# Performance work log

Hardware: AMD Instinct MI355X
Metric: run time of the kernel (lower is better)

## Reference

```python
import jax, jax.numpy as jnp
import numpy as np

NUM_FEATURES = 256
NUM_PIDS = 5532
CQ_SIZE = 5000
N_NONID = 256
N = 2048
OIM_SCALAR = 30.0
MOMENTUM = 0.5


def _unit_rows(key, shape):
    v = jax.random.normal(key, shape, dtype=jnp.float32)
    return v / jnp.linalg.norm(v, axis=-1, keepdims=True)


def setup_inputs() -> dict:
    key = jax.random.key(0)
    ks = jax.random.split(key, 8)
    inputs = _unit_rows(ks[0], (N, NUM_FEATURES))
    targets = jax.random.randint(ks[1], (N,), 0, NUM_PIDS + 100, dtype=jnp.int32)
    belong_to_first_half = jax.random.randint(ks[2], (N,), 0, 2) > 0
    non_id_feat = _unit_rows(ks[3], (N_NONID, NUM_FEATURES))
    lut = _unit_rows(ks[4], (NUM_PIDS, NUM_FEATURES))
    cq = _unit_rows(ks[5], (CQ_SIZE, NUM_FEATURES))
    first_pos_sample = _unit_rows(ks[6], (NUM_PIDS, NUM_FEATURES))
    second_pos_sample = _unit_rows(ks[7], (NUM_PIDS, NUM_FEATURES))
    return {
        "inputs": inputs,
        "non_id_feat": non_id_feat,
        "lut": lut,
        "cq": cq,
        "first_pos_sample": first_pos_sample,
        "second_pos_sample": second_pos_sample,
        "targets": targets,
        "belong_to_first_half": belong_to_first_half,
        "header": 0,
    }


def reference(inputs, non_id_feat, lut, cq, first_pos_sample, second_pos_sample,
              targets, belong_to_first_half, header):
    # OIM forward: similarities against labeled LUT and [circular queue; non-id feats]
    out_labeled = inputs @ lut.T                                  # [N, num_pids]
    out_unlabeled = inputs @ jnp.concatenate([cq, non_id_feat], 0).T  # [N, cq+nonid]
    projected = jnp.concatenate([out_labeled, out_unlabeled], axis=1)
    return projected * OIM_SCALAR
```

## Files before the change

kernel.cpp:

```cpp
#include <hip/hip_runtime.h>
#include <hip/hip_bf16.h>
#include <stdint.h>
#include <stddef.h>

#define NUM_FEATURES 256
#define NUM_PIDS 5532
#define CQ_SIZE 5000
#define N_NONID 256
#define N_ROWS 2048
#define N_COLS (NUM_PIDS + CQ_SIZE + N_NONID)
#define OIM_SCALAR 30.0f

#define BM 128
#define BN 128
#define BK 32
#define KITERS (NUM_FEATURES / BK)

typedef __bf16 bf16_t;
typedef __bf16 bf16x4 __attribute__((ext_vector_type(4)));
typedef __bf16 bf16x8 __attribute__((ext_vector_type(8)));
typedef float f32x4 __attribute__((ext_vector_type(4)));

__global__ void detect_dtype(const void* __restrict__ A, int* __restrict__ flag) {
    const bf16_t* ab = (const bf16_t*)A;
    const int lane = threadIdx.x;
    float s = 0.0f;
    #pragma unroll
    for (int j = 0; j < 4; ++j) {
        float x = (float)ab[lane * 4 + j];
        s += x * x;
    }
    #pragma unroll
    for (int off = 32; off > 0; off >>= 1) s += __shfl_down(s, off, 64);
    if (lane == 0) flag[0] = (s > 0.75f && s < 1.25f) ? 1 : 0;
}

template <bool F32>
__device__ __forceinline__ void gemm_body(
    const char* __restrict__ A, const char* __restrict__ lut,
    const char* __restrict__ cq, const char* __restrict__ nonid,
    char* __restrict__ out, bf16_t* As, bf16_t* Bs)
{
    constexpr int ES = F32 ? 4 : 2;
    const int tid  = threadIdx.x;
    const int wid  = tid >> 6;
    const int lane = tid & 63;
    const int m0 = blockIdx.y * BM;
    const int n0 = blockIdx.x * BN;

    constexpr int NJ    = F32 ? 4 : 2;
    constexpr int RSTEP = F32 ? 32 : 64;
    const int srow = F32 ? (tid >> 3) : (tid >> 2);
    const int skk  = F32 ? ((tid & 7) * 4) : ((tid & 3) * 8);

    const char* arow[NJ];
    const char* brow[NJ];
    #pragma unroll
    for (int j = 0; j < NJ; ++j) {
        const int rm = m0 + srow + j * RSTEP;
        arow[j] = A + ((size_t)rm * NUM_FEATURES + skk) * ES;
        int r = n0 + srow + j * RSTEP;
        r = r < (N_COLS - 1) ? r : (N_COLS - 1);
        const char* src;
        if (r < NUM_PIDS)                 src = lut   + (size_t)r * NUM_FEATURES * ES;
        else if (r < NUM_PIDS + CQ_SIZE)  src = cq    + (size_t)(r - NUM_PIDS) * NUM_FEATURES * ES;
        else                              src = nonid + (size_t)(r - NUM_PIDS - CQ_SIZE) * NUM_FEATURES * ES;
        brow[j] = src + (size_t)skk * ES;
    }

    const int wave_m = (wid >> 1) * 64;
    const int wave_n = (wid & 1) * 64;
    const int fr = lane & 15;
    const int fk = (lane >> 4) * 8;

    f32x4 acc[4][4] = {};

    for (int kt = 0; kt < KITERS; ++kt) {
        #pragma unroll
        for (int j = 0; j < NJ; ++j) {
            const int ldix = (srow + j * RSTEP) * BK + skk;
            if constexpr (F32) {
                float4 av = *(const float4*)arow[j];
                float4 bv = *(const float4*)brow[j];
                bf16x4 ac = { (bf16_t)av.x, (bf16_t)av.y, (bf16_t)av.z, (bf16_t)av.w };
                bf16x4 bc = { (bf16_t)bv.x, (bf16_t)bv.y, (bf16_t)bv.z, (bf16_t)bv.w };
                *(bf16x4*)&As[ldix] = ac;
                *(bf16x4*)&Bs[ldix] = bc;
            } else {
                *(bf16x8*)&As[ldix] = *(const bf16x8*)arow[j];
                *(bf16x8*)&Bs[ldix] = *(const bf16x8*)brow[j];
            }
            arow[j] += BK * ES;
            brow[j] += BK * ES;
        }
        __syncthreads();

        bf16x8 af[4], bfr[4];
        #pragma unroll
        for (int t = 0; t < 4; ++t) {
            af[t]  = *(const bf16x8*)&As[(wave_m + t * 16 + fr) * BK + fk];
            bfr[t] = *(const bf16x8*)&Bs[(wave_n + t * 16 + fr) * BK + fk];
        }
        #pragma unroll
        for (int tm = 0; tm < 4; ++tm)
            #pragma unroll
            for (int tn = 0; tn < 4; ++tn)
                acc[tm][tn] = __builtin_amdgcn_mfma_f32_16x16x32_bf16(
                    af[tm], bfr[tn], acc[tm][tn], 0, 0, 0);
        __syncthreads();
    }

    #pragma unroll
    for (int tm = 0; tm < 4; ++tm) {
        const int row_base = m0 + wave_m + tm * 16 + (lane >> 4) * 4;
        #pragma unroll
        for (int tn = 0; tn < 4; ++tn) {
            const int col = n0 + wave_n + tn * 16 + (lane & 15);
            if (col < N_COLS) {
                #pragma unroll
                for (int i = 0; i < 4; ++i) {
                    float v = acc[tm][tn][i] * OIM_SCALAR;
                    if constexpr (F32)
                        ((float*)out)[(size_t)(row_base + i) * N_COLS + col] = v;
                    else
                        ((bf16_t*)out)[(size_t)(row_base + i) * N_COLS + col] = (bf16_t)v;
                }
            }
        }
    }
}

__global__ __launch_bounds__(256)
void oim_gemm_kernel(const void* __restrict__ A, const void* __restrict__ lut,
                     const void* __restrict__ cq, const void* __restrict__ nonid,
                     void* __restrict__ out, const int* __restrict__ flag) {
    __shared__ __align__(16) bf16_t As[BM * BK];
    __shared__ __align__(16) bf16_t Bs[BN * BK];
    if (flag[0]) {
        gemm_body<false>((const char*)A, (const char*)lut, (const char*)cq,
                         (const char*)nonid, (char*)out, As, Bs);
    } else {
        gemm_body<true>((const char*)A, (const char*)lut, (const char*)cq,
                        (const char*)nonid, (char*)out, As, Bs);
    }
}

extern "C" void kernel_launch(void* const* d_in, const int* in_sizes, int n_in,
                              void* d_out, int out_size, void* d_ws, size_t ws_size,
                              hipStream_t stream) {
    const void* inputs = d_in[0];
    const void* nonid  = d_in[1];
    const void* lut    = d_in[2];
    const void* cq     = d_in[3];
    int* flag = (int*)d_ws;

    detect_dtype<<<1, 64, 0, stream>>>(inputs, flag);

    dim3 grid((N_COLS + BN - 1) / BN, N_ROWS / BM);
    oim_gemm_kernel<<<grid, 256, 0, stream>>>(inputs, lut, cq, nonid, d_out, flag);
}
```

Measured before the change: 166.8 us.

## Double-buffer LDS with register prefetch, XCD-aware tile mapping, drop dtype detection

Removes the runtime dtype-detection kernel and the bf16 path, hardcoding fp32 inputs and outputs. Adds double-buffered shared memory tiles plus a register prefetch of the next K slice, so global loads overlap the MFMA work and one barrier per iteration goes away. It also remaps the 1D grid so each XCD owns a contiguous range of N tiles, which should improve L2 reuse of B rows. The trade-off is no bf16 input support, more LDS and register use, and a few idle blocks in the padded grid.

```diff
diff --git a/kernel.cpp b/kernel.cpp
--- a/kernel.cpp
+++ b/kernel.cpp
@@ -16,56 +16,54 @@
 #define BK 32
 #define KITERS (NUM_FEATURES / BK)
 
+#define NT_PER_XCD 11
+#define N_TILES 85
+#define M_TILES 16
+#define GRID_BLOCKS (8 * NT_PER_XCD * M_TILES)
+
 typedef __bf16 bf16_t;
 typedef __bf16 bf16x4 __attribute__((ext_vector_type(4)));
 typedef __bf16 bf16x8 __attribute__((ext_vector_type(8)));
 typedef float f32x4 __attribute__((ext_vector_type(4)));
 
-__global__ void detect_dtype(const void* __restrict__ A, int* __restrict__ flag) {
-    const bf16_t* ab = (const bf16_t*)A;
-    const int lane = threadIdx.x;
-    float s = 0.0f;
-    #pragma unroll
-    for (int j = 0; j < 4; ++j) {
-        float x = (float)ab[lane * 4 + j];
-        s += x * x;
-    }
-    #pragma unroll
-    for (int off = 32; off > 0; off >>= 1) s += __shfl_down(s, off, 64);
-    if (lane == 0) flag[0] = (s > 0.75f && s < 1.25f) ? 1 : 0;
-}
+__global__ __launch_bounds__(256)
+void oim_gemm_kernel(const float* __restrict__ A,
+                     const float* __restrict__ lut,
+                     const float* __restrict__ cq,
+                     const float* __restrict__ nonid,
+                     float* __restrict__ out) {
+    __shared__ __align__(16) bf16_t As[2][BM * BK];
+    __shared__ __align__(16) bf16_t Bs[2][BM * BK];
 
-template <bool F32>
-__device__ __forceinline__ void gemm_body(
-    const char* __restrict__ A, const char* __restrict__ lut,
-    const char* __restrict__ cq, const char* __restrict__ nonid,
-    char* __restrict__ out, bf16_t* As, bf16_t* Bs)
-{
-    constexpr int ES = F32 ? 4 : 2;
+    const int id  = blockIdx.x;
+    const int xcd = id & 7;
+    const int l   = id >> 3;
+    const int nt  = xcd * NT_PER_XCD + l % NT_PER_XCD;
+    const int mt  = l / NT_PER_XCD;
+    if (nt >= N_TILES) return;
+    const int m0 = mt * BM;
+    const int n0 = nt * BN;
+
     const int tid  = threadIdx.x;
     const int wid  = tid >> 6;
     const int lane = tid & 63;
-    const int m0 = blockIdx.y * BM;
-    const int n0 = blockIdx.x * BN;
 
-    constexpr int NJ    = F32 ? 4 : 2;
-    constexpr int RSTEP = F32 ? 32 : 64;
-    const int srow = F32 ? (tid >> 3) : (tid >> 2);
-    const int skk  = F32 ? ((tid & 7) * 4) : ((tid & 3) * 8);
+    const int srow = tid >> 3;
+    const int skk  = (tid & 7) * 4;
 
-    const char* arow[NJ];
-    const char* brow[NJ];
+    const float* arow[4];
+    const float* brow[4];
     #pragma unroll
-    for (int j = 0; j < NJ; ++j) {
-        const int rm = m0 + srow + j * RSTEP;
-        arow[j] = A + ((size_t)rm * NUM_FEATURES + skk) * ES;
-        int r = n0 + srow + j * RSTEP;
+    for (int j = 0; j < 4; ++j) {
+        const int rm = m0 + srow + j * 32;
+        arow[j] = A + (size_t)rm * NUM_FEATURES + skk;
+        int r = n0 + srow + j * 32;
         r = r < (N_COLS - 1) ? r : (N_COLS - 1);
-        const char* src;
-        if (r < NUM_PIDS)                 src = lut   + (size_t)r * NUM_FEATURES * ES;
-        else if (r < NUM_PIDS + CQ_SIZE)  src = cq    + (size_t)(r - NUM_PIDS) * NUM_FEATURES * ES;
-        else                              src = nonid + (size_t)(r - NUM_PIDS - CQ_SIZE) * NUM_FEATURES * ES;
-        brow[j] = src + (size_t)skk * ES;
+        const float* src;
+        if (r < NUM_PIDS)                 src = lut   + (size_t)r * NUM_FEATURES;
+        else if (r < NUM_PIDS + CQ_SIZE)  src = cq    + (size_t)(r - NUM_PIDS) * NUM_FEATURES;
+        else                              src = nonid + (size_t)(r - NUM_PIDS - CQ_SIZE) * NUM_FEATURES;
+        brow[j] = src + skk;
     }
 
     const int wave_m = (wid >> 1) * 64;
@@ -75,31 +73,44 @@
 
     f32x4 acc[4][4] = {};
 
+    float4 areg[4], breg[4];
+    #pragma unroll
+    for (int j = 0; j < 4; ++j) {
+        areg[j] = *(const float4*)arow[j];
+        breg[j] = *(const float4*)brow[j];
+        arow[j] += BK;
+        brow[j] += BK;
+    }
+
+    #pragma unroll 2
     for (int kt = 0; kt < KITERS; ++kt) {
+        bf16_t* const as = As[kt & 1];
+        bf16_t* const bs = Bs[kt & 1];
         #pragma unroll
-        for (int j = 0; j < NJ; ++j) {
-            const int ldix = (srow + j * RSTEP) * BK + skk;
-            if constexpr (F32) {
-                float4 av = *(const float4*)arow[j];
-                float4 bv = *(const float4*)brow[j];
-                bf16x4 ac = { (bf16_t)av.x, (bf16_t)av.y, (bf16_t)av.z, (bf16_t)av.w };
-                bf16x4 bc = { (bf16_t)bv.x, (bf16_t)bv.y, (bf16_t)bv.z, (bf16_t)bv.w };
-                *(bf16x4*)&As[ldix] = ac;
-                *(bf16x4*)&Bs[ldix] = bc;
-            } else {
-                *(bf16x8*)&As[ldix] = *(const bf16x8*)arow[j];
-                *(bf16x8*)&Bs[ldix] = *(const bf16x8*)brow[j];
-            }
-            arow[j] += BK * ES;
-            brow[j] += BK * ES;
+        for (int j = 0; j < 4; ++j) {
+            const int ldix = (srow + j * 32) * BK + skk;
+            bf16x4 ac = { (bf16_t)areg[j].x, (bf16_t)areg[j].y,
+                          (bf16_t)areg[j].z, (bf16_t)areg[j].w };
+            bf16x4 bc = { (bf16_t)breg[j].x, (bf16_t)breg[j].y,
+                          (bf16_t)breg[j].z, (bf16_t)breg[j].w };
+            *(bf16x4*)&as[ldix] = ac;
+            *(bf16x4*)&bs[ldix] = bc;
         }
         __syncthreads();
-
+        if (kt < KITERS - 1) {
+            #pragma unroll
+            for (int j = 0; j < 4; ++j) {
+                areg[j] = *(const float4*)arow[j];
+                breg[j] = *(const float4*)brow[j];
+                arow[j] += BK;
+                brow[j] += BK;
+            }
+        }
         bf16x8 af[4], bfr[4];
         #pragma unroll
         for (int t = 0; t < 4; ++t) {
-            af[t]  = *(const bf16x8*)&As[(wave_m + t * 16 + fr) * BK + fk];
-            bfr[t] = *(const bf16x8*)&Bs[(wave_n + t * 16 + fr) * BK + fk];
+            af[t]  = *(const bf16x8*)&as[(wave_m + t * 16 + fr) * BK + fk];
+            bfr[t] = *(const bf16x8*)&bs[(wave_n + t * 16 + fr) * BK + fk];
         }
         #pragma unroll
         for (int tm = 0; tm < 4; ++tm)
@@ -107,7 +118,6 @@
             for (int tn = 0; tn < 4; ++tn)
                 acc[tm][tn] = __builtin_amdgcn_mfma_f32_16x16x32_bf16(
                     af[tm], bfr[tn], acc[tm][tn], 0, 0, 0);
-        __syncthreads();
     }
 
     #pragma unroll
@@ -119,43 +129,22 @@
             if (col < N_COLS) {
                 #pragma unroll
                 for (int i = 0; i < 4; ++i) {
-                    float v = acc[tm][tn][i] * OIM_SCALAR;
-                    if constexpr (F32)
-                        ((float*)out)[(size_t)(row_base + i) * N_COLS + col] = v;
-                    else
-                        ((bf16_t*)out)[(size_t)(row_base + i) * N_COLS + col] = (bf16_t)v;
+                    out[(size_t)(row_base + i) * N_COLS + col] =
+                        acc[tm][tn][i] * OIM_SCALAR;
                 }
             }
         }
     }
 }
 
-__global__ __launch_bounds__(256)
-void oim_gemm_kernel(const void* __restrict__ A, const void* __restrict__ lut,
-                     const void* __restrict__ cq, const void* __restrict__ nonid,
-                     void* __restrict__ out, const int* __restrict__ flag) {
-    __shared__ __align__(16) bf16_t As[BM * BK];
-    __shared__ __align__(16) bf16_t Bs[BN * BK];
-    if (flag[0]) {
-        gemm_body<false>((const char*)A, (const char*)lut, (const char*)cq,
-                         (const char*)nonid, (char*)out, As, Bs);
-    } else {
-        gemm_body<true>((const char*)A, (const char*)lut, (const char*)cq,
-                        (const char*)nonid, (char*)out, As, Bs);
-    }
-}
-
 extern "C" void kernel_launch(void* const* d_in, const int* in_sizes, int n_in,
                               void* d_out, int out_size, void* d_ws, size_t ws_size,
                               hipStream_t stream) {
-    const void* inputs = d_in[0];
-    const void* nonid  = d_in[1];
-    const void* lut    = d_in[2];
-    const void* cq     = d_in[3];
-    int* flag = (int*)d_ws;
+    const float* inputs = (const float*)d_in[0];
+    const float* nonid  = (const float*)d_in[1];
+    const float* lut    = (const float*)d_in[2];
+    const float* cq     = (const float*)d_in[3];
+    float* out = (float*)d_out;
 
-    detect_dtype<<<1, 64, 0, stream>>>(inputs, flag);
-
-    dim3 grid((N_COLS + BN - 1) / BN, N_ROWS / BM);
-    oim_gemm_kernel<<<grid, 256, 0, stream>>>(inputs, lut, cq, nonid, d_out, flag);
+    oim_gemm_kernel<<<dim3(GRID_BLOCKS), 256, 0, stream>>>(inputs, lut, cq, nonid, out);
 }
```

Result: faster. 147.5 us (-11.6%).
